# Optimization experiments

Measured on AMD Instinct MI355X. Metric: run time of the kernel, lower is better.

## Reference

```python
import jax, jax.numpy as jnp
import numpy as np

B = 2048      # batch
IN = 784      # input_dim (28*28, hardcoded by x.view(-1,28,28))
H = 512       # hidden_dim
OUT = 512     # output_dim
E = 8         # n_experts
ER = 4        # n_recurrent (experts 0..3 are LSTM experts)
ES = E - ER   # simple MLP experts
T = 28        # LSTM timesteps
F = 28        # LSTM input features per step
K = 5         # n_active = max(1, int(8*0.7))
TEMP = 2.718281828459045  # np.e


def setup_inputs() -> dict:
    key = jax.random.key(0)
    ks = jax.random.split(key, 14)
    s = 0.05
    return {
        "x":    jax.random.normal(ks[0], (B, IN), dtype=jnp.float32),
        # Boltzmann gate
        "Wg":   jax.random.normal(ks[1], (E, IN), dtype=jnp.float32) * s,
        "bg":   jnp.zeros((E,), dtype=jnp.float32),
        # Recurrent experts (stacked over ER): PyTorch LSTM layout, gate order i,f,g,o
        "Wih":  jax.random.normal(ks[2], (ER, 4 * H, F), dtype=jnp.float32) * s,
        "Whh":  jax.random.normal(ks[3], (ER, 4 * H, H), dtype=jnp.float32) * s,
        "bih":  jnp.zeros((ER, 4 * H), dtype=jnp.float32),
        "bhh":  jnp.zeros((ER, 4 * H), dtype=jnp.float32),
        "fcW":  jax.random.normal(ks[4], (ER, OUT, H), dtype=jnp.float32) * s,
        "fcb":  jnp.zeros((ER, OUT), dtype=jnp.float32),
        # Simple experts (stacked over ES)
        "W1":   jax.random.normal(ks[5], (ES, H, IN), dtype=jnp.float32) * s,
        "b1":   jnp.zeros((ES, H), dtype=jnp.float32),
        "W2":   jax.random.normal(ks[6], (ES, OUT, H), dtype=jnp.float32) * s,
        "b2":   jnp.zeros((ES, OUT), dtype=jnp.float32),
    }


def _forward(x, Wg, bg, Wih, Whh, bih, bhh, fcW, fcb, W1, b1, W2, b2):
    # --- Boltzmann gate: softmax(scores/T), top-k mask, renormalize ---
    scores = (x @ Wg.T + bg) / TEMP                    # [B,E]
    probs = jax.nn.softmax(scores, axis=-1)
    _, idx = jax.lax.top_k(probs, K)                   # [B,K]
    mask = jax.nn.one_hot(idx, E, dtype=probs.dtype).sum(axis=-2)  # [B,E]
    w = probs * mask
    weights = w / (w.sum(axis=-1, keepdims=True) + 1e-8)

    # --- Recurrent experts (vectorized over ER, scan over time) ---
    xs = x.reshape(B, T, F)
    xs_t = jnp.transpose(xs, (1, 0, 2))                # [T,B,F]

    def step(carry, x_t):
        h, c = carry                                   # each [ER,B,H]
        gates = (jnp.einsum('bi,egi->ebg', x_t, Wih) + bih[:, None, :]
                 + jnp.einsum('ebh,egh->ebg', h, Whh) + bhh[:, None, :])  # [ER,B,4H]
        i_g = jax.nn.sigmoid(gates[..., 0 * H:1 * H])
        f_g = jax.nn.sigmoid(gates[..., 1 * H:2 * H])
        g_g = jnp.tanh(gates[..., 2 * H:3 * H])
        o_g = jax.nn.sigmoid(gates[..., 3 * H:4 * H])
        c = f_g * c + i_g * g_g
        h = o_g * jnp.tanh(c)
        return (h, c), None

    h0 = jnp.zeros((ER, B, H), dtype=x.dtype)
    (h_last, _), _ = jax.lax.scan(step, (h0, h0), xs_t)
    rec_out = jnp.einsum('ebh,eoh->ebo', h_last, fcW) + fcb[:, None, :]   # [ER,B,OUT]

    # --- Simple experts (dropout is identity at eval) ---
    h1 = jax.nn.relu(jnp.einsum('bi,ehi->ebh', x, W1) + b1[:, None, :])   # [ES,B,H]
    simp_out = jnp.einsum('ebh,eoh->ebo', h1, W2) + b2[:, None, :]        # [ES,B,OUT]

    expert_outputs = jnp.concatenate([rec_out, simp_out], axis=0)         # [E,B,OUT]
    return jnp.einsum('be,ebo->bo', weights, expert_outputs)              # [B,OUT]


def reference(x, Wg, bg, Wih, Whh, bih, bhh, fcW, fcb, W1, b1, W2, b2):
    return _forward(x, Wg, bg, Wih, Whh, bih, bhh, fcW, fcb, W1, b1, W2, b2)
```

## Files before the change

kernel.cpp:

```cpp
#include <hip/hip_runtime.h>
#include <stdint.h>

#define CDIV(a,b) (((a)+(b)-1)/(b))

typedef unsigned short u16;
using bf16x8   = __attribute__((ext_vector_type(8))) short;
using floatx4  = __attribute__((ext_vector_type(4))) float;
using floatx16 = __attribute__((ext_vector_type(16))) float;

constexpr int B_N   = 2048;
constexpr int IN_N  = 784;
constexpr int H_N   = 512;
constexpr int OUT_N = 512;
constexpr int E_N   = 8;
constexpr int ER_N  = 4;
constexpr int ES_N  = 4;
constexpr int T_N   = 28;
constexpr int F_N   = 28;
constexpr int G4H   = 2048;
constexpr int KA    = 544;
constexpr int KB8   = KA / 8;
constexpr int NKI   = KA / 16;
constexpr int XP    = 800;

__device__ __forceinline__ u16 f2bf(float f) {
  union { float f; uint32_t u; } v; v.f = f;
  uint32_t r = v.u + 0x7fffu + ((v.u >> 16) & 1u);
  return (u16)(r >> 16);
}
__device__ __forceinline__ float sigm(float x) {
  return __builtin_amdgcn_rcpf(1.f + __expf(-x));
}
__device__ __forceinline__ float tanhf_(float x) {
  return __builtin_fmaf(-2.f, __builtin_amdgcn_rcpf(__expf(2.f * x) + 1.f), 1.f);
}

__device__ __forceinline__ void async16(const void* g, void* l) {
  __builtin_amdgcn_global_load_lds(
      (__attribute__((address_space(1))) void*)g,
      (__attribute__((address_space(3))) void*)l, 16, 0, 0);
}

__global__ __launch_bounds__(512, 2)
void lstm_persist(const u16* __restrict__ Wc, const float* __restrict__ brec,
                  const u16* __restrict__ xb, u16* __restrict__ A0,
                  u16* __restrict__ A1, u16* __restrict__ Hlast,
                  int* __restrict__ Gbar)
{
  extern __shared__ __align__(16) u16 Ws[];
  const int tid  = threadIdx.x;
  const int lane = tid & 63;
  const int wave = tid >> 6;
  const int blk  = blockIdx.x;
  const int xcd  = blk & 7;
  const int i8   = blk >> 3;
  const int nt   = i8 & 15;
  const int g    = (i8 >> 4) * 8 + xcd;
  const int z    = g >> 2;
  const int mr   = g & 3;
  const int ln   = lane & 31;
  const int hw   = lane >> 5;
  const int gslot = g * 64;

  {
    const u16* Wsrc = Wc + (size_t)(z * 16 + nt) * (4 * KB8 * 256);
    const int base = wave * (17 * 512);
#pragma unroll
    for (int it = 0; it < 17; ++it)
      async16(Wsrc + base + it * 512 + lane * 8, Ws + base + it * 512);
  }

  float bb[4];
#pragma unroll
  for (int j = 0; j < 4; ++j)
    bb[j] = brec[((z * 16 + nt) * 4 + j) * 32 + ln];

  float c[2][16];
#pragma unroll
  for (int i = 0; i < 2; ++i)
#pragma unroll
    for (int r = 0; r < 16; ++r) c[i][r] = 0.f;

  const int mblk0 = mr * 16 + wave * 2;
  const int hcol  = nt * 32 + ln;
  const size_t zoff = (size_t)z * ((size_t)64 * KB8 * 256);
  __syncthreads();

  for (int t = 0; t < T_N; ++t) {
    const u16* Az  = ((t & 1) ? A1 : A0) + zoff;
    u16*       Aoz = ((t & 1) ? A0 : A1) + zoff;

    const u16* Ap0 = Az + ((size_t)mblk0 * KB8 + hw) * 256 + ln * 8;
    const u16* Ap1 = Az + ((size_t)(mblk0 + 1) * KB8 + hw) * 256 + ln * 8;

    bf16x8 pa0[2], pa1[2];
    pa0[0] = *(const bf16x8*)Ap0;          pa1[0] = *(const bf16x8*)Ap1;
    pa0[1] = *(const bf16x8*)(Ap0 + 512);  pa1[1] = *(const bf16x8*)(Ap1 + 512);

    floatx16 acc[2][4];
#pragma unroll
    for (int i = 0; i < 2; ++i)
#pragma unroll
      for (int j = 0; j < 4; ++j)
#pragma unroll
        for (int r = 0; r < 16; ++r)
          acc[i][j][r] = bb[j];

#pragma unroll 2
    for (int kk = 0; kk < NKI; ++kk) {
      bf16x8 a0 = pa0[kk & 1], a1 = pa1[kk & 1];
      if (kk + 2 < NKI) {
        pa0[kk & 1] = *(const bf16x8*)(Ap0 + (size_t)(kk + 2) * 512);
        pa1[kk & 1] = *(const bf16x8*)(Ap1 + (size_t)(kk + 2) * 512);
      }
      const u16* Bp = Ws + (2 * kk + hw) * 256 + ln * 8;
      bf16x8 b0 = *(const bf16x8*)(Bp);
      bf16x8 b1 = *(const bf16x8*)(Bp + 1 * KB8 * 256);
      bf16x8 b2 = *(const bf16x8*)(Bp + 2 * KB8 * 256);
      bf16x8 b3 = *(const bf16x8*)(Bp + 3 * KB8 * 256);
      acc[0][0] = __builtin_amdgcn_mfma_f32_32x32x16_bf16(a0, b0, acc[0][0], 0, 0, 0);
      acc[0][1] = __builtin_amdgcn_mfma_f32_32x32x16_bf16(a0, b1, acc[0][1], 0, 0, 0);
      acc[0][2] = __builtin_amdgcn_mfma_f32_32x32x16_bf16(a0, b2, acc[0][2], 0, 0, 0);
      acc[0][3] = __builtin_amdgcn_mfma_f32_32x32x16_bf16(a0, b3, acc[0][3], 0, 0, 0);
      acc[1][0] = __builtin_amdgcn_mfma_f32_32x32x16_bf16(a1, b0, acc[1][0], 0, 0, 0);
      acc[1][1] = __builtin_amdgcn_mfma_f32_32x32x16_bf16(a1, b1, acc[1][1], 0, 0, 0);
      acc[1][2] = __builtin_amdgcn_mfma_f32_32x32x16_bf16(a1, b2, acc[1][2], 0, 0, 0);
      acc[1][3] = __builtin_amdgcn_mfma_f32_32x32x16_bf16(a1, b3, acc[1][3], 0, 0, 0);
    }

    const int last = (t == T_N - 1);
#pragma unroll
    for (int i = 0; i < 2; ++i) {
      const int mb = mblk0 + i;
#pragma unroll
      for (int r = 0; r < 16; ++r) {
        float cv = sigm(acc[i][1][r]) * c[i][r]
                 + sigm(acc[i][0][r]) * tanhf_(acc[i][2][r]);
        c[i][r] = cv;
        u16 hb = f2bf(sigm(acc[i][3][r]) * tanhf_(cv));
        int mrow = 4 * hw + (r & 3) + 8 * (r >> 2);
        if (!last)
          __builtin_nontemporal_store(hb,
              &Aoz[((size_t)mb * KB8 + (hcol >> 3)) * 256 + mrow * 8 + (hcol & 7)]);
        else
          Hlast[((size_t)(z * B_N + mb * 32 + mrow)) * H_N + hcol] = hb;
      }
    }

    if (t + 1 < T_N) {
      for (int idx = nt * 512 + tid; idx < 512 * F_N; idx += 16 * 512) {
        int ml  = idx / F_N, col = idx - ml * F_N;
        int m   = mr * 512 + ml;
        int k   = H_N + col;
        __builtin_nontemporal_store(xb[(size_t)m * XP + (t + 1) * F_N + col],
            &Aoz[((size_t)(m >> 5) * KB8 + (k >> 3)) * 256 + (m & 31) * 8 + (k & 7)]);
      }

      __syncthreads();
      if (tid == 0) {
        __hip_atomic_fetch_add(&Gbar[gslot], 1, __ATOMIC_RELEASE,
                               __HIP_MEMORY_SCOPE_AGENT);
        const int target = 16 * (t + 1);
        while (__hip_atomic_load(&Gbar[gslot], __ATOMIC_RELAXED,
                                 __HIP_MEMORY_SCOPE_AGENT) < target)
          __builtin_amdgcn_s_sleep(1);
        __builtin_amdgcn_fence(__ATOMIC_ACQUIRE, "agent");
      }
      __syncthreads();
    }
  }
}

template<int RELU, int OBF>
__global__ __launch_bounds__(256, 2)
void gemm_bt(const u16* __restrict__ A, int lda, long sAz,
             const u16* __restrict__ Bw, int ldb, long sBz,
             const float* __restrict__ bias, int sBiz,
             void* __restrict__ Cv, int ldc, long sCz,
             int K)
{
  __shared__ __align__(16) u16 As[128 * 32];
  __shared__ __align__(16) u16 Bs[128 * 32];
  const int tid  = threadIdx.x;
  const int lane = tid & 63;
  const int wave = tid >> 6;
  const int m0 = blockIdx.y * 128;
  const int n0 = blockIdx.x * 128;
  const int z  = blockIdx.z;
  const u16* Ab = A  + (size_t)z * sAz;
  const u16* Bb = Bw + (size_t)z * sBz;

  const int wm   = (wave & 1) * 64;
  const int wn   = (wave >> 1) * 64;
  const int lm   = lane & 15;
  const int quad = lane >> 4;

  const int s0 = wave * 64 + lane;
  const int r0 = s0 >> 2, c0 = (s0 & 3) * 8;
  const int s1 = s0 + 256;
  const int r1 = s1 >> 2, c1 = (s1 & 3) * 8;

  floatx4 acc[4][4] = {};

  for (int k0 = 0; k0 < K; k0 += 32) {
    async16(Ab + (size_t)(m0 + r0) * lda + (k0 + c0), As + wave * 512);
    async16(Ab + (size_t)(m0 + r1) * lda + (k0 + c1), As + 2048 + wave * 512);
    async16(Bb + (size_t)(n0 + r0) * ldb + (k0 + c0), Bs + wave * 512);
    async16(Bb + (size_t)(n0 + r1) * ldb + (k0 + c1), Bs + 2048 + wave * 512);
    __syncthreads();
    bf16x8 af[4], bf_[4];
#pragma unroll
    for (int i = 0; i < 4; ++i)
      af[i] = *(const bf16x8*)&As[(wm + i * 16 + lm) * 32 + quad * 8];
#pragma unroll
    for (int j = 0; j < 4; ++j)
      bf_[j] = *(const bf16x8*)&Bs[(wn + j * 16 + lm) * 32 + quad * 8];
#pragma unroll
    for (int i = 0; i < 4; ++i)
#pragma unroll
      for (int j = 0; j < 4; ++j)
        acc[i][j] = __builtin_amdgcn_mfma_f32_16x16x32_bf16(af[i], bf_[j], acc[i][j], 0, 0, 0);
    __syncthreads();
  }

  float bj[4];
#pragma unroll
  for (int j = 0; j < 4; ++j)
    bj[j] = bias ? bias[z * sBiz + n0 + wn + j * 16 + lm] : 0.f;

#pragma unroll
  for (int i = 0; i < 4; ++i) {
#pragma unroll
    for (int r = 0; r < 4; ++r) {
      int m = m0 + wm + i * 16 + quad * 4 + r;
      size_t row = (size_t)z * sCz + (size_t)m * ldc;
#pragma unroll
      for (int j = 0; j < 4; ++j) {
        int n = n0 + wn + j * 16 + lm;
        float v = acc[i][j][r] + bj[j];
        if (RELU) v = fmaxf(v, 0.f);
        if (OBF) ((u16*)Cv)[row + n] = f2bf(v);
        else     ((float*)Cv)[row + n] = v;
      }
    }
  }
}

__global__ __launch_bounds__(256)
void gate_k(const float* __restrict__ x, const float* __restrict__ Wg,
            const float* __restrict__ bg, float* __restrict__ Wt)
{
  int lane = threadIdx.x & 63;
  int row  = blockIdx.x * 4 + (threadIdx.x >> 6);
  float ps[E_N];
#pragma unroll
  for (int e = 0; e < E_N; ++e) ps[e] = 0.f;
  const float* xr = x + (size_t)row * IN_N;
  for (int k = lane; k < IN_N; k += 64) {
    float xv = xr[k];
#pragma unroll
    for (int e = 0; e < E_N; ++e) ps[e] += xv * Wg[e * IN_N + k];
  }
#pragma unroll
  for (int e = 0; e < E_N; ++e) {
#pragma unroll
    for (int off = 32; off >= 1; off >>= 1) ps[e] += __shfl_down(ps[e], off);
  }
  if (lane == 0) {
    float s[E_N], mx = -1e30f;
#pragma unroll
    for (int e = 0; e < E_N; ++e) { s[e] = (ps[e] + bg[e]) * 0.36787944117144233f; mx = fmaxf(mx, s[e]); }
    float pr[E_N], sum = 0.f;
#pragma unroll
    for (int e = 0; e < E_N; ++e) { pr[e] = __expf(s[e] - mx); sum += pr[e]; }
    float inv = 1.f / sum;
#pragma unroll
    for (int e = 0; e < E_N; ++e) pr[e] *= inv;
    unsigned used = 0; float wsum = 0.f;
    for (int k = 0; k < 5; ++k) {
      int am = -1; float bv = -1.f;
      for (int e = 0; e < E_N; ++e)
        if (!((used >> e) & 1) && pr[e] > bv) { bv = pr[e]; am = e; }
      used |= 1u << am; wsum += pr[am];
    }
    float winv = 1.f / (wsum + 1e-8f);
    for (int e = 0; e < E_N; ++e)
      Wt[row * E_N + e] = ((used >> e) & 1) ? pr[e] * winv : 0.f;
  }
}

__global__ __launch_bounds__(256)
void combine_k(const float* __restrict__ O, const float* __restrict__ Wt, float* __restrict__ out)
{
  int idx = blockIdx.x * 256 + threadIdx.x;
  if (idx >= B_N * OUT_N) return;
  int b = idx / OUT_N;
  float a = 0.f;
#pragma unroll
  for (int e = 0; e < E_N; ++e)
    a += Wt[b * E_N + e] * O[(size_t)e * B_N * OUT_N + idx];
  out[idx] = a;
}

__global__ void prep_x_k(const float* __restrict__ x, u16* __restrict__ xb) {
  int idx = blockIdx.x * 256 + threadIdx.x;
  if (idx >= B_N * XP) return;
  int k = idx % XP, b = idx / XP;
  xb[idx] = f2bf(k < IN_N ? x[(size_t)b * IN_N + k] : 0.f);
}
__global__ void prep_wfrag_k(const float* __restrict__ Whh, const float* __restrict__ Wih,
                             u16* __restrict__ Wc) {
  int idx = blockIdx.x * 256 + threadIdx.x;
  if (idx >= ER_N * G4H * KA) return;
  int e8 = idx & 7, ln = (idx >> 3) & 31;
  int k8 = (idx >> 8) % KB8;
  int rest = (idx >> 8) / KB8;
  int j = rest & 3, nt = (rest >> 2) & 15, z = rest >> 6;
  int h = nt * 32 + ln, k = k8 * 8 + e8;
  int g = j * H_N + h;
  float v = 0.f;
  if (k < H_N)            v = Whh[((size_t)(z * G4H + g)) * H_N + k];
  else if (k < H_N + F_N) v = Wih[((size_t)(z * G4H + g)) * F_N + (k - H_N)];
  Wc[idx] = f2bf(v);
}
__global__ void prep_bfrag_k(const float* __restrict__ bih, const float* __restrict__ bhh,
                             float* __restrict__ o) {
  int idx = blockIdx.x * 256 + threadIdx.x;
  if (idx >= ER_N * G4H) return;
  int ln = idx & 31, j = (idx >> 5) & 3, nt = (idx >> 7) & 15, z = idx >> 11;
  int g = z * G4H + j * H_N + nt * 32 + ln;
  o[idx] = bih[g] + bhh[g];
}
__global__ void cvt_k(const float* __restrict__ in, u16* __restrict__ o, int n) {
  int idx = blockIdx.x * 256 + threadIdx.x;
  if (idx < n) o[idx] = f2bf(in[idx]);
}
__global__ void prep_w1_k(const float* __restrict__ W1, u16* __restrict__ o) {
  int idx = blockIdx.x * 256 + threadIdx.x;
  if (idx >= ES_N * H_N * XP) return;
  int k = idx % XP; int r = idx / XP;
  o[idx] = f2bf(k < IN_N ? W1[(size_t)r * IN_N + k] : 0.f);
}
__global__ void init_Afrag_k(u16* __restrict__ A0, u16* __restrict__ A1,
                             const u16* __restrict__ xb) {
  int idx = blockIdx.x * 256 + threadIdx.x;
  if (idx >= ER_N * B_N * KA) return;
  int e8 = idx & 7, mrow = (idx >> 3) & 31;
  int k8 = (idx >> 8) % KB8;
  int mb = ((idx >> 8) / KB8) & 63;
  int k = k8 * 8 + e8, m = mb * 32 + mrow;
  u16 v = 0;
  if (k >= H_N && k < H_N + F_N) v = xb[(size_t)m * XP + (k - H_N)];
  A0[idx] = v;
  A1[idx] = 0;
}
__global__ void zero_i_k(int* __restrict__ p, int n) {
  int i = blockIdx.x * 256 + threadIdx.x;
  if (i < n) p[i] = 0;
}

extern "C" void kernel_launch(void* const* d_in, const int* in_sizes, int n_in,
                              void* d_out, int out_size, void* d_ws, size_t ws_size,
                              hipStream_t stream) {
  const float* x   = (const float*)d_in[0];
  const float* Wg  = (const float*)d_in[1];
  const float* bg  = (const float*)d_in[2];
  const float* Wih = (const float*)d_in[3];
  const float* Whh = (const float*)d_in[4];
  const float* bih = (const float*)d_in[5];
  const float* bhh = (const float*)d_in[6];
  const float* fcW = (const float*)d_in[7];
  const float* fcb = (const float*)d_in[8];
  const float* W1  = (const float*)d_in[9];
  const float* b1  = (const float*)d_in[10];
  const float* W2  = (const float*)d_in[11];
  const float* b2  = (const float*)d_in[12];
  float* out = (float*)d_out;

  char* p = (char*)d_ws;
  auto take = [&](size_t bytes) { void* q = (void*)p; p += (bytes + 255) & ~(size_t)255; return q; };
  u16*   xb    = (u16*)  take((size_t)B_N * XP * 2);
  u16*   Wc    = (u16*)  take((size_t)ER_N * G4H * KA * 2);
  float* brec  = (float*)take((size_t)ER_N * G4H * 4);
  u16*   Wcomb = (u16*)  take((size_t)E_N * OUT_N * H_N * 2);
  u16*   W1b   = (u16*)  take((size_t)ES_N * H_N * XP * 2);
  u16*   A0    = (u16*)  take((size_t)ER_N * B_N * KA * 2);
  u16*   A1    = (u16*)  take((size_t)ER_N * B_N * KA * 2);
  u16*   Hcomb = (u16*)  take((size_t)E_N * B_N * H_N * 2);
  float* bcomb = (float*)take((size_t)E_N * OUT_N * 4);
  float* Ob    = (float*)take((size_t)E_N * B_N * OUT_N * 4);
  float* Wgt   = (float*)take((size_t)B_N * E_N * 4);
  int*   Gbar  = (int*)  take((size_t)16 * 64 * 4);

  u16* Hlast = Hcomb;
  u16* H1    = Hcomb + (size_t)ER_N * B_N * H_N;

  dim3 blk(256);
  prep_x_k    <<<CDIV(B_N * XP, 256),           blk, 0, stream>>>(x, xb);
  prep_wfrag_k<<<CDIV(ER_N * G4H * KA, 256),    blk, 0, stream>>>(Whh, Wih, Wc);
  prep_bfrag_k<<<CDIV(ER_N * G4H, 256),         blk, 0, stream>>>(bih, bhh, brec);
  cvt_k       <<<CDIV(ER_N * OUT_N * H_N, 256), blk, 0, stream>>>(fcW, Wcomb, ER_N * OUT_N * H_N);
  cvt_k       <<<CDIV(ES_N * OUT_N * H_N, 256), blk, 0, stream>>>(
      W2, Wcomb + (size_t)ER_N * OUT_N * H_N, ES_N * OUT_N * H_N);
  prep_w1_k   <<<CDIV(ES_N * H_N * XP, 256),    blk, 0, stream>>>(W1, W1b);
  init_Afrag_k<<<CDIV(ER_N * B_N * KA, 256),    blk, 0, stream>>>(A0, A1, xb);
  zero_i_k    <<<CDIV(16 * 64, 256),            blk, 0, stream>>>(Gbar, 16 * 64);
  gate_k      <<<B_N / 4,                       blk, 0, stream>>>(x, Wg, bg, Wgt);
  hipMemcpyAsync(bcomb, fcb, (size_t)ER_N * OUT_N * 4,
                 hipMemcpyDeviceToDevice, stream);
  hipMemcpyAsync(bcomb + (size_t)ER_N * OUT_N, b2, (size_t)ES_N * OUT_N * 4,
                 hipMemcpyDeviceToDevice, stream);

  gemm_bt<1, 1><<<dim3(H_N / 128, B_N / 128, ES_N), blk, 0, stream>>>(
      xb, XP, 0L,
      W1b, XP, (long)H_N * XP,
      b1, H_N,
      (void*)H1, H_N, (long)B_N * H_N, XP);

  constexpr unsigned ldsBytes = 4u * KB8 * 256u * 2u;
  hipFuncSetAttribute((const void*)lstm_persist,
                      hipFuncAttributeMaxDynamicSharedMemorySize, ldsBytes);
  {
    const u16* a_Wc = Wc; const float* a_br = brec; const u16* a_xb = xb;
    u16* a_A0 = A0; u16* a_A1 = A1; u16* a_Hl = Hlast; int* a_gb = Gbar;
    void* args[] = {(void*)&a_Wc, (void*)&a_br, (void*)&a_xb,
                    (void*)&a_A0, (void*)&a_A1, (void*)&a_Hl, (void*)&a_gb};
    hipLaunchCooperativeKernel((const void*)lstm_persist, dim3(256), dim3(512),
                               args, ldsBytes, stream);
  }

  gemm_bt<0, 0><<<dim3(OUT_N / 128, B_N / 128, E_N), blk, 0, stream>>>(
      Hcomb, H_N, (long)B_N * H_N,
      Wcomb, H_N, (long)OUT_N * H_N,
      bcomb, OUT_N,
      (void*)Ob, OUT_N, (long)B_N * OUT_N, H_N);

  combine_k<<<CDIV(B_N * OUT_N, 256), blk, 0, stream>>>(Ob, Wgt, out);
}
```

Baseline: 941.2 us.

## Use 16 waves per LSTM block with one M-tile per wave

The persistent LSTM kernel now launches 1024 threads per block instead of 512. Each wave handles one 32-row M block instead of two, which halves the accumulator and cell-state registers per wave and doubles the number of waves available to hide latency. The weight preload and the x-scatter loops are re-strided to cover the larger thread count. The trade-off is that each B-fragment read from LDS is reused across only one A tile instead of two, so LDS traffic per MFMA doubles. The __launch_bounds__(1024, 4) setting may also force register spilling.

```diff
diff --git a/kernel.cpp b/kernel.cpp
--- a/kernel.cpp
+++ b/kernel.cpp
@@ -41,7 +41,7 @@
       (__attribute__((address_space(3))) void*)l, 16, 0, 0);
 }
 
-__global__ __launch_bounds__(512, 2)
+__global__ __launch_bounds__(1024, 4)
 void lstm_persist(const u16* __restrict__ Wc, const float* __restrict__ brec,
                   const u16* __restrict__ xb, u16* __restrict__ A0,
                   u16* __restrict__ A1, u16* __restrict__ Hlast,
@@ -64,10 +64,8 @@
 
   {
     const u16* Wsrc = Wc + (size_t)(z * 16 + nt) * (4 * KB8 * 256);
-    const int base = wave * (17 * 512);
-#pragma unroll
-    for (int it = 0; it < 17; ++it)
-      async16(Wsrc + base + it * 512 + lane * 8, Ws + base + it * 512);
+    for (int off = tid * 8; off < 4 * KB8 * 256; off += 1024 * 8)
+      async16(Wsrc + off, Ws + off);
   }
 
   float bb[4];
@@ -75,14 +73,12 @@
   for (int j = 0; j < 4; ++j)
     bb[j] = brec[((z * 16 + nt) * 4 + j) * 32 + ln];
 
-  float c[2][16];
-#pragma unroll
-  for (int i = 0; i < 2; ++i)
-#pragma unroll
-    for (int r = 0; r < 16; ++r) c[i][r] = 0.f;
-
-  const int mblk0 = mr * 16 + wave * 2;
-  const int hcol  = nt * 32 + ln;
+  float c[16];
+#pragma unroll
+  for (int r = 0; r < 16; ++r) c[r] = 0.f;
+
+  const int mblk = mr * 16 + wave;
+  const int hcol = nt * 32 + ln;
   const size_t zoff = (size_t)z * ((size_t)64 * KB8 * 256);
   __syncthreads();
 
@@ -90,65 +86,51 @@
     const u16* Az  = ((t & 1) ? A1 : A0) + zoff;
     u16*       Aoz = ((t & 1) ? A0 : A1) + zoff;
 
-    const u16* Ap0 = Az + ((size_t)mblk0 * KB8 + hw) * 256 + ln * 8;
-    const u16* Ap1 = Az + ((size_t)(mblk0 + 1) * KB8 + hw) * 256 + ln * 8;
-
-    bf16x8 pa0[2], pa1[2];
-    pa0[0] = *(const bf16x8*)Ap0;          pa1[0] = *(const bf16x8*)Ap1;
-    pa0[1] = *(const bf16x8*)(Ap0 + 512);  pa1[1] = *(const bf16x8*)(Ap1 + 512);
-
-    floatx16 acc[2][4];
-#pragma unroll
-    for (int i = 0; i < 2; ++i)
-#pragma unroll
-      for (int j = 0; j < 4; ++j)
-#pragma unroll
-        for (int r = 0; r < 16; ++r)
-          acc[i][j][r] = bb[j];
+    const u16* Ap = Az + ((size_t)mblk * KB8 + hw) * 256 + ln * 8;
+
+    bf16x8 pa[2];
+    pa[0] = *(const bf16x8*)Ap;
+    pa[1] = *(const bf16x8*)(Ap + 512);
+
+    floatx16 acc[4];
+#pragma unroll
+    for (int j = 0; j < 4; ++j)
+#pragma unroll
+      for (int r = 0; r < 16; ++r)
+        acc[j][r] = bb[j];
 
 #pragma unroll 2
     for (int kk = 0; kk < NKI; ++kk) {
-      bf16x8 a0 = pa0[kk & 1], a1 = pa1[kk & 1];
-      if (kk + 2 < NKI) {
-        pa0[kk & 1] = *(const bf16x8*)(Ap0 + (size_t)(kk + 2) * 512);
-        pa1[kk & 1] = *(const bf16x8*)(Ap1 + (size_t)(kk + 2) * 512);
-      }
+      bf16x8 a = pa[kk & 1];
+      if (kk + 2 < NKI)
+        pa[kk & 1] = *(const bf16x8*)(Ap + (size_t)(kk + 2) * 512);
       const u16* Bp = Ws + (2 * kk + hw) * 256 + ln * 8;
       bf16x8 b0 = *(const bf16x8*)(Bp);
       bf16x8 b1 = *(const bf16x8*)(Bp + 1 * KB8 * 256);
       bf16x8 b2 = *(const bf16x8*)(Bp + 2 * KB8 * 256);
       bf16x8 b3 = *(const bf16x8*)(Bp + 3 * KB8 * 256);
-      acc[0][0] = __builtin_amdgcn_mfma_f32_32x32x16_bf16(a0, b0, acc[0][0], 0, 0, 0);
-      acc[0][1] = __builtin_amdgcn_mfma_f32_32x32x16_bf16(a0, b1, acc[0][1], 0, 0, 0);
-      acc[0][2] = __builtin_amdgcn_mfma_f32_32x32x16_bf16(a0, b2, acc[0][2], 0, 0, 0);
-      acc[0][3] = __builtin_amdgcn_mfma_f32_32x32x16_bf16(a0, b3, acc[0][3], 0, 0, 0);
-      acc[1][0] = __builtin_amdgcn_mfma_f32_32x32x16_bf16(a1, b0, acc[1][0], 0, 0, 0);
-      acc[1][1] = __builtin_amdgcn_mfma_f32_32x32x16_bf16(a1, b1, acc[1][1], 0, 0, 0);
-      acc[1][2] = __builtin_amdgcn_mfma_f32_32x32x16_bf16(a1, b2, acc[1][2], 0, 0, 0);
-      acc[1][3] = __builtin_amdgcn_mfma_f32_32x32x16_bf16(a1, b3, acc[1][3], 0, 0, 0);
+      acc[0] = __builtin_amdgcn_mfma_f32_32x32x16_bf16(a, b0, acc[0], 0, 0, 0);
+      acc[1] = __builtin_amdgcn_mfma_f32_32x32x16_bf16(a, b1, acc[1], 0, 0, 0);
+      acc[2] = __builtin_amdgcn_mfma_f32_32x32x16_bf16(a, b2, acc[2], 0, 0, 0);
+      acc[3] = __builtin_amdgcn_mfma_f32_32x32x16_bf16(a, b3, acc[3], 0, 0, 0);
     }
 
     const int last = (t == T_N - 1);
 #pragma unroll
-    for (int i = 0; i < 2; ++i) {
-      const int mb = mblk0 + i;
-#pragma unroll
-      for (int r = 0; r < 16; ++r) {
-        float cv = sigm(acc[i][1][r]) * c[i][r]
-                 + sigm(acc[i][0][r]) * tanhf_(acc[i][2][r]);
-        c[i][r] = cv;
-        u16 hb = f2bf(sigm(acc[i][3][r]) * tanhf_(cv));
-        int mrow = 4 * hw + (r & 3) + 8 * (r >> 2);
-        if (!last)
-          __builtin_nontemporal_store(hb,
-              &Aoz[((size_t)mb * KB8 + (hcol >> 3)) * 256 + mrow * 8 + (hcol & 7)]);
-        else
-          Hlast[((size_t)(z * B_N + mb * 32 + mrow)) * H_N + hcol] = hb;
-      }
+    for (int r = 0; r < 16; ++r) {
+      float cv = sigm(acc[1][r]) * c[r] + sigm(acc[0][r]) * tanhf_(acc[2][r]);
+      c[r] = cv;
+      u16 hb = f2bf(sigm(acc[3][r]) * tanhf_(cv));
+      int mrow = 4 * hw + (r & 3) + 8 * (r >> 2);
+      if (!last)
+        __builtin_nontemporal_store(hb,
+            &Aoz[((size_t)mblk * KB8 + (hcol >> 3)) * 256 + mrow * 8 + (hcol & 7)]);
+      else
+        Hlast[((size_t)(z * B_N + mblk * 32 + mrow)) * H_N + hcol] = hb;
     }
 
     if (t + 1 < T_N) {
-      for (int idx = nt * 512 + tid; idx < 512 * F_N; idx += 16 * 512) {
+      for (int idx = nt * 1024 + tid; idx < 512 * F_N; idx += 16 * 1024) {
         int ml  = idx / F_N, col = idx - ml * F_N;
         int m   = mr * 512 + ml;
         int k   = H_N + col;
@@ -425,7 +407,7 @@
     u16* a_A0 = A0; u16* a_A1 = A1; u16* a_Hl = Hlast; int* a_gb = Gbar;
     void* args[] = {(void*)&a_Wc, (void*)&a_br, (void*)&a_xb,
                     (void*)&a_A0, (void*)&a_A1, (void*)&a_Hl, (void*)&a_gb};
-    hipLaunchCooperativeKernel((const void*)lstm_persist, dim3(256), dim3(512),
+    hipLaunchCooperativeKernel((const void*)lstm_persist, dim3(256), dim3(1024),
                                args, ldsBytes, stream);
   }
 
```

After: 0.9997 ms. +6.2%, slower.

## Separate LSTM input projection into pre-fragmented Xf buffer and skip h at t=0

Applied to the files above, without the earlier changes.

The per-step input features move out of the shared A buffers into a dedicated pre-laid-out Xf array, built once by a new prep kernel. Inside the persistent LSTM kernel they are loaded straight into registers before the grid barrier, replacing the scatter of x values into A. The A buffers shrink to hidden-only width and the init_Afrag kernel is removed. At t=0 the recurrent MFMA loop is skipped because h is zero. This cuts per-step global stores and A traffic and overlaps the x loads with the barrier, at the cost of more code paths in the hot loop and an extra prep kernel.

```diff
diff --git a/kernel.cpp b/kernel.cpp
--- a/kernel.cpp
+++ b/kernel.cpp
@@ -20,7 +20,8 @@
 constexpr int G4H   = 2048;
 constexpr int KA    = 544;
 constexpr int KB8   = KA / 8;
-constexpr int NKI   = KA / 16;
+constexpr int HB8   = 64;
+constexpr int NH    = 32;
 constexpr int XP    = 800;
 
 __device__ __forceinline__ u16 f2bf(float f) {
@@ -43,7 +44,7 @@
 
 __global__ __launch_bounds__(512, 2)
 void lstm_persist(const u16* __restrict__ Wc, const float* __restrict__ brec,
-                  const u16* __restrict__ xb, u16* __restrict__ A0,
+                  const u16* __restrict__ Xf, u16* __restrict__ A0,
                   u16* __restrict__ A1, u16* __restrict__ Hlast,
                   int* __restrict__ Gbar)
 {
@@ -64,10 +65,8 @@
 
   {
     const u16* Wsrc = Wc + (size_t)(z * 16 + nt) * (4 * KB8 * 256);
-    const int base = wave * (17 * 512);
-#pragma unroll
-    for (int it = 0; it < 17; ++it)
-      async16(Wsrc + base + it * 512 + lane * 8, Ws + base + it * 512);
+    for (int off = tid * 8; off < 4 * KB8 * 256; off += 512 * 8)
+      async16(Wsrc + off, Ws + off);
   }
 
   float bb[4];
@@ -83,19 +82,25 @@
 
   const int mblk0 = mr * 16 + wave * 2;
   const int hcol  = nt * 32 + ln;
-  const size_t zoff = (size_t)z * ((size_t)64 * KB8 * 256);
+  const size_t zoff = (size_t)z * ((size_t)64 * HB8 * 256);
+
+  bf16x8 pa0[2], pa1[2];
+  {
+    const u16* X0 = Xf + ((size_t)0 * 64 + mblk0) * 1024 + hw * 256 + ln * 8;
+    const u16* X1 = Xf + ((size_t)0 * 64 + mblk0 + 1) * 1024 + hw * 256 + ln * 8;
+    pa0[0] = *(const bf16x8*)X0;          pa1[0] = *(const bf16x8*)X1;
+    pa0[1] = *(const bf16x8*)(X0 + 512);  pa1[1] = *(const bf16x8*)(X1 + 512);
+  }
   __syncthreads();
 
   for (int t = 0; t < T_N; ++t) {
     const u16* Az  = ((t & 1) ? A1 : A0) + zoff;
     u16*       Aoz = ((t & 1) ? A0 : A1) + zoff;
 
-    const u16* Ap0 = Az + ((size_t)mblk0 * KB8 + hw) * 256 + ln * 8;
-    const u16* Ap1 = Az + ((size_t)(mblk0 + 1) * KB8 + hw) * 256 + ln * 8;
-
-    bf16x8 pa0[2], pa1[2];
-    pa0[0] = *(const bf16x8*)Ap0;          pa1[0] = *(const bf16x8*)Ap1;
-    pa0[1] = *(const bf16x8*)(Ap0 + 512);  pa1[1] = *(const bf16x8*)(Ap1 + 512);
+    const u16* Ap0 = Az + ((size_t)mblk0 * HB8 + hw) * 256 + ln * 8;
+    const u16* Ap1 = Az + ((size_t)(mblk0 + 1) * HB8 + hw) * 256 + ln * 8;
+
+    const int nh = (t == 0) ? 0 : NH;
 
     floatx16 acc[2][4];
 #pragma unroll
@@ -106,14 +111,10 @@
         for (int r = 0; r < 16; ++r)
           acc[i][j][r] = bb[j];
 
-#pragma unroll 2
-    for (int kk = 0; kk < NKI; ++kk) {
-      bf16x8 a0 = pa0[kk & 1], a1 = pa1[kk & 1];
-      if (kk + 2 < NKI) {
-        pa0[kk & 1] = *(const bf16x8*)(Ap0 + (size_t)(kk + 2) * 512);
-        pa1[kk & 1] = *(const bf16x8*)(Ap1 + (size_t)(kk + 2) * 512);
-      }
-      const u16* Bp = Ws + (2 * kk + hw) * 256 + ln * 8;
+    {
+      bf16x8 a0 = pa0[0], a1 = pa1[0];
+      if (nh > 0) { pa0[0] = *(const bf16x8*)Ap0; pa1[0] = *(const bf16x8*)Ap1; }
+      const u16* Bp = Ws + (64 + hw) * 256 + ln * 8;
       bf16x8 b0 = *(const bf16x8*)(Bp);
       bf16x8 b1 = *(const bf16x8*)(Bp + 1 * KB8 * 256);
       bf16x8 b2 = *(const bf16x8*)(Bp + 2 * KB8 * 256);
@@ -127,6 +128,48 @@
       acc[1][2] = __builtin_amdgcn_mfma_f32_32x32x16_bf16(a1, b2, acc[1][2], 0, 0, 0);
       acc[1][3] = __builtin_amdgcn_mfma_f32_32x32x16_bf16(a1, b3, acc[1][3], 0, 0, 0);
     }
+    {
+      bf16x8 a0 = pa0[1], a1 = pa1[1];
+      if (nh > 1) {
+        pa0[1] = *(const bf16x8*)(Ap0 + 512);
+        pa1[1] = *(const bf16x8*)(Ap1 + 512);
+      }
+      const u16* Bp = Ws + (66 + hw) * 256 + ln * 8;
+      bf16x8 b0 = *(const bf16x8*)(Bp);
+      bf16x8 b1 = *(const bf16x8*)(Bp + 1 * KB8 * 256);
+      bf16x8 b2 = *(const bf16x8*)(Bp + 2 * KB8 * 256);
+      bf16x8 b3 = *(const bf16x8*)(Bp + 3 * KB8 * 256);
+      acc[0][0] = __builtin_amdgcn_mfma_f32_32x32x16_bf16(a0, b0, acc[0][0], 0, 0, 0);
+      acc[0][1] = __builtin_amdgcn_mfma_f32_32x32x16_bf16(a0, b1, acc[0][1], 0, 0, 0);
+      acc[0][2] = __builtin_amdgcn_mfma_f32_32x32x16_bf16(a0, b2, acc[0][2], 0, 0, 0);
+      acc[0][3] = __builtin_amdgcn_mfma_f32_32x32x16_bf16(a0, b3, acc[0][3], 0, 0, 0);
+      acc[1][0] = __builtin_amdgcn_mfma_f32_32x32x16_bf16(a1, b0, acc[1][0], 0, 0, 0);
+      acc[1][1] = __builtin_amdgcn_mfma_f32_32x32x16_bf16(a1, b1, acc[1][1], 0, 0, 0);
+      acc[1][2] = __builtin_amdgcn_mfma_f32_32x32x16_bf16(a1, b2, acc[1][2], 0, 0, 0);
+      acc[1][3] = __builtin_amdgcn_mfma_f32_32x32x16_bf16(a1, b3, acc[1][3], 0, 0, 0);
+    }
+
+#pragma unroll 2
+    for (int j = 0; j < nh; ++j) {
+      bf16x8 a0 = pa0[j & 1], a1 = pa1[j & 1];
+      if (j + 2 < nh) {
+        pa0[j & 1] = *(const bf16x8*)(Ap0 + (size_t)(j + 2) * 512);
+        pa1[j & 1] = *(const bf16x8*)(Ap1 + (size_t)(j + 2) * 512);
+      }
+      const u16* Bp = Ws + (2 * j + hw) * 256 + ln * 8;
+      bf16x8 b0 = *(const bf16x8*)(Bp);
+      bf16x8 b1 = *(const bf16x8*)(Bp + 1 * KB8 * 256);
+      bf16x8 b2 = *(const bf16x8*)(Bp + 2 * KB8 * 256);
+      bf16x8 b3 = *(const bf16x8*)(Bp + 3 * KB8 * 256);
+      acc[0][0] = __builtin_amdgcn_mfma_f32_32x32x16_bf16(a0, b0, acc[0][0], 0, 0, 0);
+      acc[0][1] = __builtin_amdgcn_mfma_f32_32x32x16_bf16(a0, b1, acc[0][1], 0, 0, 0);
+      acc[0][2] = __builtin_amdgcn_mfma_f32_32x32x16_bf16(a0, b2, acc[0][2], 0, 0, 0);
+      acc[0][3] = __builtin_amdgcn_mfma_f32_32x32x16_bf16(a0, b3, acc[0][3], 0, 0, 0);
+      acc[1][0] = __builtin_amdgcn_mfma_f32_32x32x16_bf16(a1, b0, acc[1][0], 0, 0, 0);
+      acc[1][1] = __builtin_amdgcn_mfma_f32_32x32x16_bf16(a1, b1, acc[1][1], 0, 0, 0);
+      acc[1][2] = __builtin_amdgcn_mfma_f32_32x32x16_bf16(a1, b2, acc[1][2], 0, 0, 0);
+      acc[1][3] = __builtin_amdgcn_mfma_f32_32x32x16_bf16(a1, b3, acc[1][3], 0, 0, 0);
+    }
 
     const int last = (t == T_N - 1);
 #pragma unroll
@@ -141,20 +184,17 @@
         int mrow = 4 * hw + (r & 3) + 8 * (r >> 2);
         if (!last)
           __builtin_nontemporal_store(hb,
-              &Aoz[((size_t)mb * KB8 + (hcol >> 3)) * 256 + mrow * 8 + (hcol & 7)]);
+              &Aoz[((size_t)mb * HB8 + (hcol >> 3)) * 256 + mrow * 8 + (hcol & 7)]);
         else
           Hlast[((size_t)(z * B_N + mb * 32 + mrow)) * H_N + hcol] = hb;
       }
     }
 
     if (t + 1 < T_N) {
-      for (int idx = nt * 512 + tid; idx < 512 * F_N; idx += 16 * 512) {
-        int ml  = idx / F_N, col = idx - ml * F_N;
-        int m   = mr * 512 + ml;
-        int k   = H_N + col;
-        __builtin_nontemporal_store(xb[(size_t)m * XP + (t + 1) * F_N + col],
-            &Aoz[((size_t)(m >> 5) * KB8 + (k >> 3)) * 256 + (m & 31) * 8 + (k & 7)]);
-      }
+      const u16* X0 = Xf + ((size_t)(t + 1) * 64 + mblk0) * 1024 + hw * 256 + ln * 8;
+      const u16* X1 = Xf + ((size_t)(t + 1) * 64 + mblk0 + 1) * 1024 + hw * 256 + ln * 8;
+      pa0[0] = *(const bf16x8*)X0;          pa1[0] = *(const bf16x8*)X1;
+      pa0[1] = *(const bf16x8*)(X0 + 512);  pa1[1] = *(const bf16x8*)(X1 + 512);
 
       __syncthreads();
       if (tid == 0) {
@@ -308,6 +348,17 @@
   int k = idx % XP, b = idx / XP;
   xb[idx] = f2bf(k < IN_N ? x[(size_t)b * IN_N + k] : 0.f);
 }
+__global__ void prep_xfrag_k(const float* __restrict__ x, u16* __restrict__ Xf) {
+  int idx = blockIdx.x * 256 + threadIdx.x;
+  if (idx >= T_N * B_N * 32) return;
+  int e8 = idx & 7, mrow = (idx >> 3) & 31;
+  int k8 = (idx >> 8) & 3;
+  int mb = (idx >> 10) & 63;
+  int t  = idx >> 16;
+  int m = mb * 32 + mrow, col = k8 * 8 + e8;
+  float v = (col < F_N) ? x[(size_t)m * IN_N + t * F_N + col] : 0.f;
+  Xf[idx] = f2bf(v);
+}
 __global__ void prep_wfrag_k(const float* __restrict__ Whh, const float* __restrict__ Wih,
                              u16* __restrict__ Wc) {
   int idx = blockIdx.x * 256 + threadIdx.x;
@@ -340,19 +391,6 @@
   if (idx >= ES_N * H_N * XP) return;
   int k = idx % XP; int r = idx / XP;
   o[idx] = f2bf(k < IN_N ? W1[(size_t)r * IN_N + k] : 0.f);
-}
-__global__ void init_Afrag_k(u16* __restrict__ A0, u16* __restrict__ A1,
-                             const u16* __restrict__ xb) {
-  int idx = blockIdx.x * 256 + threadIdx.x;
-  if (idx >= ER_N * B_N * KA) return;
-  int e8 = idx & 7, mrow = (idx >> 3) & 31;
-  int k8 = (idx >> 8) % KB8;
-  int mb = ((idx >> 8) / KB8) & 63;
-  int k = k8 * 8 + e8, m = mb * 32 + mrow;
-  u16 v = 0;
-  if (k >= H_N && k < H_N + F_N) v = xb[(size_t)m * XP + (k - H_N)];
-  A0[idx] = v;
-  A1[idx] = 0;
 }
 __global__ void zero_i_k(int* __restrict__ p, int n) {
   int i = blockIdx.x * 256 + threadIdx.x;
@@ -382,10 +420,11 @@
   u16*   xb    = (u16*)  take((size_t)B_N * XP * 2);
   u16*   Wc    = (u16*)  take((size_t)ER_N * G4H * KA * 2);
   float* brec  = (float*)take((size_t)ER_N * G4H * 4);
+  u16*   Xf    = (u16*)  take((size_t)T_N * B_N * 32 * 2);
   u16*   Wcomb = (u16*)  take((size_t)E_N * OUT_N * H_N * 2);
   u16*   W1b   = (u16*)  take((size_t)ES_N * H_N * XP * 2);
-  u16*   A0    = (u16*)  take((size_t)ER_N * B_N * KA * 2);
-  u16*   A1    = (u16*)  take((size_t)ER_N * B_N * KA * 2);
+  u16*   A0    = (u16*)  take((size_t)ER_N * B_N * H_N * 2);
+  u16*   A1    = (u16*)  take((size_t)ER_N * B_N * H_N * 2);
   u16*   Hcomb = (u16*)  take((size_t)E_N * B_N * H_N * 2);
   float* bcomb = (float*)take((size_t)E_N * OUT_N * 4);
   float* Ob    = (float*)take((size_t)E_N * B_N * OUT_N * 4);
@@ -397,13 +436,13 @@
 
   dim3 blk(256);
   prep_x_k    <<<CDIV(B_N * XP, 256),           blk, 0, stream>>>(x, xb);
+  prep_xfrag_k<<<CDIV(T_N * B_N * 32, 256),     blk, 0, stream>>>(x, Xf);
   prep_wfrag_k<<<CDIV(ER_N * G4H * KA, 256),    blk, 0, stream>>>(Whh, Wih, Wc);
   prep_bfrag_k<<<CDIV(ER_N * G4H, 256),         blk, 0, stream>>>(bih, bhh, brec);
   cvt_k       <<<CDIV(ER_N * OUT_N * H_N, 256), blk, 0, stream>>>(fcW, Wcomb, ER_N * OUT_N * H_N);
   cvt_k       <<<CDIV(ES_N * OUT_N * H_N, 256), blk, 0, stream>>>(
       W2, Wcomb + (size_t)ER_N * OUT_N * H_N, ES_N * OUT_N * H_N);
   prep_w1_k   <<<CDIV(ES_N * H_N * XP, 256),    blk, 0, stream>>>(W1, W1b);
-  init_Afrag_k<<<CDIV(ER_N * B_N * KA, 256),    blk, 0, stream>>>(A0, A1, xb);
   zero_i_k    <<<CDIV(16 * 64, 256),            blk, 0, stream>>>(Gbar, 16 * 64);
   gate_k      <<<B_N / 4,                       blk, 0, stream>>>(x, Wg, bg, Wgt);
   hipMemcpyAsync(bcomb, fcb, (size_t)ER_N * OUT_N * 4,
@@ -421,9 +460,9 @@
   hipFuncSetAttribute((const void*)lstm_persist,
                       hipFuncAttributeMaxDynamicSharedMemorySize, ldsBytes);
   {
-    const u16* a_Wc = Wc; const float* a_br = brec; const u16* a_xb = xb;
+    const u16* a_Wc = Wc; const float* a_br = brec; const u16* a_Xf = Xf;
     u16* a_A0 = A0; u16* a_A1 = A1; u16* a_Hl = Hlast; int* a_gb = Gbar;
-    void* args[] = {(void*)&a_Wc, (void*)&a_br, (void*)&a_xb,
+    void* args[] = {(void*)&a_Wc, (void*)&a_br, (void*)&a_Xf,
                     (void*)&a_A0, (void*)&a_A1, (void*)&a_Hl, (void*)&a_gb};
     hipLaunchCooperativeKernel((const void*)lstm_persist, dim3(256), dim3(512),
                                args, ldsBytes, stream);
```

After: 1.401 ms. 1.49x slower.
